# Kernel optimization log

Hardware: AMD Instinct MI355X
Metric: run time of the kernel (lower is better)

Reference implementation:

```python
import jax, jax.numpy as jnp
import numpy as np

GROUPS = 32
EPS = 1e-5


def group_norm(x, gamma, beta):
    # x: [B,H,W,C], channels_last, groups over channel dim (Keras GroupNormalization default)
    B, H, W, C = x.shape
    xg = x.reshape(B, H, W, GROUPS, C // GROUPS)
    mean = xg.mean(axis=(1, 2, 4), keepdims=True)
    var = xg.var(axis=(1, 2, 4), keepdims=True)
    xn = ((xg - mean) * jax.lax.rsqrt(var + EPS)).reshape(B, H, W, C)
    return xn * gamma + beta


def conv1x1(x, w, b):
    # 1x1 conv == per-pixel dense: [B,H,W,C] x [C,D] -> [B,H,W,D]
    return jnp.einsum('bhwc,cd->bhwd', x, w) + b


def setup_inputs() -> dict:
    key = jax.random.key(0)
    ks = jax.random.split(key, 10)
    C = 512
    s = 1.0 / np.sqrt(C)
    inp = {
        'x': jax.random.normal(ks[0], (2, 64, 64, C), dtype=jnp.float32),
        'gamma': jnp.ones((C,), jnp.float32),
        'beta': jnp.zeros((C,), jnp.float32),
        'wq': jax.random.normal(ks[1], (C, C), jnp.float32) * s,
        'bq': jnp.zeros((C,), jnp.float32),
        'wk': jax.random.normal(ks[2], (C, C), jnp.float32) * s,
        'bk': jnp.zeros((C,), jnp.float32),
        'wv': jax.random.normal(ks[3], (C, C), jnp.float32) * s,
        'bv': jnp.zeros((C,), jnp.float32),
        'wp': jax.random.normal(ks[4], (C, C), jnp.float32) * s,
        'bp': jnp.zeros((C,), jnp.float32),
    }
    return inp


def reference(x, gamma, beta, wq, bq, wk, bk, wv, bv, wp, bp):
    B, H, W, C = x.shape
    N = H * W
    xn = group_norm(x, gamma, beta)
    q = conv1x1(xn, wq, bq).reshape(B, N, C)
    k = conv1x1(xn, wk, bk).reshape(B, N, C)
    v = conv1x1(xn, wv, bv).reshape(B, N, C)
    scale = 1.0 / jnp.sqrt(jnp.asarray(C, x.dtype))
    scores = jnp.einsum('bnc,bmc->bnm', q, k) * scale  # [B,N,N]
    attn = jax.nn.softmax(scores, axis=-1)
    out = jnp.einsum('bnm,bmc->bnc', attn, v).reshape(B, H, W, C)
    return conv1x1(out, wp, bp) + x
```

## Files before the change

kernel.cpp:

```cpp
#include <hip/hip_runtime.h>
#include <hip/hip_fp16.h>

typedef _Float16 half_t;
typedef _Float16 half8 __attribute__((ext_vector_type(8)));
typedef float floatx4 __attribute__((ext_vector_type(4)));

static constexpr int BATCH = 2;
static constexpr int NSP = 4096;
static constexpr int CH = 512;
static constexpr int NQKV = 3 * CH;

static constexpr size_t OFF_STATS = 0;
static constexpr size_t OFF_ROWSUM = 512;
static constexpr size_t OFF_WQKV = 36864;
static constexpr size_t WQKV_BYTES = (size_t)NQKV * CH * 2;
static constexpr size_t OFF_WP = OFF_WQKV + WQKV_BYTES;
static constexpr size_t WP_BYTES = (size_t)CH * CH * 2;
static constexpr size_t OFF_XN = OFF_WP + WP_BYTES;
static constexpr size_t XN_BYTES = (size_t)BATCH * NSP * CH * 2;
static constexpr size_t OFF_QKV = OFF_XN + XN_BYTES;
static constexpr size_t QKV_BYTES = (size_t)BATCH * NSP * NQKV * 2;
static constexpr size_t OFF_VT = OFF_QKV + QKV_BYTES;
static constexpr size_t OFF_AO = OFF_VT + XN_BYTES;
static constexpr size_t OFF_S = OFF_AO + XN_BYTES;
static constexpr size_t S_BYTES_1 = (size_t)NSP * NSP * 2;

__device__ __forceinline__ void gld16(void* lds, const void* g) {
  __builtin_amdgcn_global_load_lds(
      (__attribute__((address_space(1))) void*)(g),
      (__attribute__((address_space(3))) void*)(lds),
      16, 0, 0);
}

__global__ void zero4(floatx4* p, long n4) {
  long i = (long)blockIdx.x * 256 + threadIdx.x;
  if (i < n4) p[i] = floatx4{0.f, 0.f, 0.f, 0.f};
}

__global__ __launch_bounds__(256) void gn_stats(const float* __restrict__ x,
                                                float* __restrict__ st) {
  int b = blockIdx.y;
  int tid = (int)threadIdx.x;
  int c0 = (tid * 4) & (CH - 1);
  int g = c0 >> 4;
  const float* base = x + (long)b * NSP * CH + (long)blockIdx.x * 16 * CH + tid * 4;
  float s = 0.f, s2 = 0.f;
#pragma unroll
  for (int it = 0; it < 8; ++it) {
    floatx4 v = *(const floatx4*)(base + (long)it * 1024);
#pragma unroll
    for (int r = 0; r < 4; ++r) { s += v[r]; s2 += v[r] * v[r]; }
  }
  __shared__ float gs[32], gs2[32];
  if (tid < 32) { gs[tid] = 0.f; gs2[tid] = 0.f; }
  __syncthreads();
  atomicAdd(&gs[g], s);
  atomicAdd(&gs2[g], s2);
  __syncthreads();
  if (tid < 32) {
    atomicAdd(&st[(b * 32 + tid) * 2], gs[tid]);
    atomicAdd(&st[(b * 32 + tid) * 2 + 1], gs2[tid]);
  }
}

__global__ void gn_finalize(float* st) {
  int bg = threadIdx.x;
  float s = st[bg * 2], s2 = st[bg * 2 + 1];
  const float inv = 1.f / 65536.f;
  float mean = s * inv;
  float var = s2 * inv - mean * mean;
  st[bg * 2] = mean;
  st[bg * 2 + 1] = rsqrtf(var + 1e-5f);
}

__global__ __launch_bounds__(256) void gn_apply(const float* __restrict__ x,
                                                const float* __restrict__ st,
                                                const float* __restrict__ gamma,
                                                const float* __restrict__ beta,
                                                half_t* __restrict__ xn) {
  long i = ((long)blockIdx.x * 256 + threadIdx.x) * 8;
  int c = (int)(i & (CH - 1));
  int b = (int)(i >> 21);
  int g = c >> 4;
  float mean = st[((b << 5) + g) * 2];
  float rstd = st[((b << 5) + g) * 2 + 1];
  floatx4 a = *(const floatx4*)(x + i);
  floatx4 d = *(const floatx4*)(x + i + 4);
  half8 o;
#pragma unroll
  for (int r = 0; r < 4; ++r) {
    o[r]     = (half_t)((a[r] - mean) * rstd * gamma[c + r] + beta[c + r]);
    o[r + 4] = (half_t)((d[r] - mean) * rstd * gamma[c + r + 4] + beta[c + r + 4]);
  }
  *(half8*)(xn + i) = o;
}

__global__ __launch_bounds__(256) void transpose_w(
    const float* __restrict__ w0, const float* __restrict__ w1,
    const float* __restrict__ w2, const float* __restrict__ w3,
    half_t* __restrict__ o0, half_t* __restrict__ o1,
    half_t* __restrict__ o2, half_t* __restrict__ o3) {
  const float* w; half_t* o;
  switch (blockIdx.z) {
    case 0: w = w0; o = o0; break;
    case 1: w = w1; o = o1; break;
    case 2: w = w2; o = o2; break;
    default: w = w3; o = o3; break;
  }
  __shared__ float t[32][33];
  int d0 = blockIdx.x * 32, c0 = blockIdx.y * 32;
  int tx = threadIdx.x & 31, ty = threadIdx.x >> 5;
#pragma unroll
  for (int i = 0; i < 4; ++i)
    t[ty + i * 8][tx] = w[(long)(c0 + ty + i * 8) * CH + d0 + tx];
  __syncthreads();
#pragma unroll
  for (int i = 0; i < 4; ++i) {
    int d = ty + i * 8;
    o[(long)(d0 + d) * CH + c0 + tx] = (half_t)t[tx][d];
  }
}

__global__ __launch_bounds__(256) void transpose_v(const half_t* __restrict__ v,
                                                   half_t* __restrict__ vt) {
  __shared__ half_t t[32][33];
  int b = blockIdx.z;
  int d0 = blockIdx.x * 32, n0 = blockIdx.y * 32;
  int tx = threadIdx.x & 31, ty = threadIdx.x >> 5;
  const half_t* vb = v + (long)b * NSP * NQKV;
  half_t* ob = vt + (long)b * NSP * CH;
#pragma unroll
  for (int i = 0; i < 4; ++i)
    t[ty + i * 8][tx] = vb[(long)(n0 + ty + i * 8) * NQKV + d0 + tx];
  __syncthreads();
#pragma unroll
  for (int i = 0; i < 4; ++i) {
    int d = ty + i * 8;
    ob[(long)(d0 + d) * NSP + n0 + tx] = t[tx][d];
  }
}

template <int BM, int BN, int BK, int EPI, int SWZ, typename OutT>
__global__ __launch_bounds__(256) void gemm_nt(
    const half_t* __restrict__ X, const half_t* __restrict__ Y,
    OutT* __restrict__ Co, const float* __restrict__ b0,
    const float* __restrict__ b1, const float* __restrict__ b2,
    const float* __restrict__ resid, float* __restrict__ rowsum,
    int M, int N, int K, int ldx, int ldy, int ldc,
    long xbs, long ybs, long cbs, float scale) {
  constexpr int SM = BM / 32;
  constexpr int SN = BN / 32;
  constexpr int ROWS = BM + BN;
  constexpr int CPR = BK / 8;
  constexpr int RPW = 64 / CPR;
  constexpr int ROUNDS = (ROWS * BK * 2) / 4096;
  constexpr int KSTEPS = BK / 32;
  static_assert(BM % (4 * RPW) == 0, "no As/Bs straddle within a round");
  __shared__ __align__(16) half_t Sh[ROWS * BK];
  half_t* As = Sh;
  half_t* Bs = Sh + BM * BK;

  const int zb = blockIdx.z;
  int bx, by;
  if (SWZ) {
    int lin = (int)(blockIdx.x + gridDim.x * blockIdx.y);
    int wmt = 256 / (int)gridDim.x;
    by = wmt * (lin >> 8) + ((lin & 255) % wmt);
    bx = (lin & 255) / wmt;
  } else {
    bx = blockIdx.x;
    by = blockIdx.y;
  }

  const half_t* Xb = X + (long)zb * xbs;
  const half_t* Yb = Y + (long)zb * ybs;
  OutT* Cb = Co + (long)zb * cbs;

  const int m0 = by * BM;
  const int n0 = bx * BN;
  const int tid = (int)threadIdx.x;
  const int wave = tid >> 6;
  const int lane = tid & 63;
  const int quad = lane >> 4;
  const int l16 = lane & 15;
  const int wm = wave >> 1;
  const int wn = wave & 1;

  floatx4 acc[SM][SN] = {};

  const int srow = lane / CPR;
  const int schunk = lane % CPR;

  for (int k0 = 0; k0 < K; k0 += BK) {
#pragma unroll
    for (int r = 0; r < ROUNDS; ++r) {
      int row = r * (4 * RPW) + wave * RPW + srow;
      int gchunk = schunk ^ (row & (CPR - 1));
      const char* src;
      if (row < BM)
        src = (const char*)(Xb + (long)(m0 + row) * ldx + k0) + gchunk * 16;
      else
        src = (const char*)(Yb + (long)(n0 + row - BM) * ldy + k0) + gchunk * 16;
      gld16((char*)Sh + (r * 4 + wave) * 1024, src);
    }
    __syncthreads();

#pragma unroll
    for (int kk = 0; kk < KSTEPS; ++kk) {
      half8 af[SM], bf[SN];
#pragma unroll
      for (int i = 0; i < SM; ++i) {
        int m = wm * (BM / 2) + i * 16 + l16;
        int cc = (kk * 4 + quad) ^ (m & (CPR - 1));
        af[i] = *(const half8*)(As + m * BK + cc * 8);
      }
#pragma unroll
      for (int j = 0; j < SN; ++j) {
        int n = wn * (BN / 2) + j * 16 + l16;
        int cc = (kk * 4 + quad) ^ (n & (CPR - 1));
        bf[j] = *(const half8*)(Bs + n * BK + cc * 8);
      }
#pragma unroll
      for (int i = 0; i < SM; ++i)
#pragma unroll
        for (int j = 0; j < SN; ++j)
          acc[i][j] = __builtin_amdgcn_mfma_f32_16x16x32_f16(af[i], bf[j], acc[i][j], 0, 0, 0);
    }
    __syncthreads();
  }

#pragma unroll
  for (int i = 0; i < SM; ++i) {
    int gmb = m0 + wm * (BM / 2) + i * 16 + quad * 4;
    float rs[4] = {0.f, 0.f, 0.f, 0.f};
    float inv[4];
    if (EPI == 4) {
#pragma unroll
      for (int r = 0; r < 4; ++r)
        inv[r] = 1.f / rowsum[(long)zb * NSP + gmb + r];
    }
#pragma unroll
    for (int j = 0; j < SN; ++j) {
      int gn = n0 + wn * (BN / 2) + j * 16 + l16;
      float bias = 0.f, sc = 1.f;
      if (EPI == 1) {
        if (gn < CH) { bias = b0[gn]; sc = scale; }
        else if (gn < 2 * CH) { bias = b1[gn - CH]; }
        else { bias = b2[gn - 2 * CH]; }
      } else if (EPI == 2) {
        bias = b0[gn];
      }
#pragma unroll
      for (int r = 0; r < 4; ++r) {
        long idx = (long)(gmb + r) * ldc + gn;
        float v = acc[i][j][r];
        if (EPI == 1) v = (v + bias) * sc;
        if (EPI == 2) v = v + bias + resid[idx];
        if (EPI == 3) { v = __expf(v); rs[r] += v; }
        if (EPI == 4) v *= inv[r];
        Cb[idx] = (OutT)v;
      }
    }
    if (EPI == 3) {
#pragma unroll
      for (int r = 0; r < 4; ++r) {
        float v = rs[r];
        v += __shfl_xor(v, 1);
        v += __shfl_xor(v, 2);
        v += __shfl_xor(v, 4);
        v += __shfl_xor(v, 8);
        if (l16 == 0) atomicAdd(&rowsum[(long)zb * NSP + gmb + r], v);
      }
    }
  }
}

extern "C" void kernel_launch(void* const* d_in, const int* in_sizes, int n_in,
                              void* d_out, int out_size, void* d_ws, size_t ws_size,
                              hipStream_t stream) {
  const float* x = (const float*)d_in[0];
  const float* gamma = (const float*)d_in[1];
  const float* beta = (const float*)d_in[2];
  const float* wq = (const float*)d_in[3];
  const float* bq = (const float*)d_in[4];
  const float* wk = (const float*)d_in[5];
  const float* bk = (const float*)d_in[6];
  const float* wv = (const float*)d_in[7];
  const float* bv = (const float*)d_in[8];
  const float* wp = (const float*)d_in[9];
  const float* bp = (const float*)d_in[10];
  float* out = (float*)d_out;
  char* ws = (char*)d_ws;

  float* st = (float*)(ws + OFF_STATS);
  float* rsum = (float*)(ws + OFF_ROWSUM);
  half_t* wqkvT = (half_t*)(ws + OFF_WQKV);
  half_t* wpT = (half_t*)(ws + OFF_WP);
  half_t* xn = (half_t*)(ws + OFF_XN);
  half_t* qkv = (half_t*)(ws + OFF_QKV);
  half_t* vt = (half_t*)(ws + OFF_VT);
  half_t* ao = (half_t*)(ws + OFF_AO);
  half_t* S = (half_t*)(ws + OFF_S);

  half_t* q = qkv;
  half_t* k = qkv + CH;
  half_t* v = qkv + 2 * CH;

  const float scale = 0.044194173824159216f;
  const long bQKV = (long)NSP * NQKV;
  const long bNC = (long)NSP * CH;
  const long bNN = (long)NSP * NSP;

  zero4<<<9, 256, 0, stream>>>((floatx4*)st, 2080);
  gn_stats<<<dim3(256, BATCH), 256, 0, stream>>>(x, st);
  gn_finalize<<<1, 64, 0, stream>>>(st);
  gn_apply<<<2048, 256, 0, stream>>>(x, st, gamma, beta, xn);
  transpose_w<<<dim3(16, 16, 4), 256, 0, stream>>>(
      wq, wk, wv, wp, wqkvT, wqkvT + (size_t)CH * CH, wqkvT + 2 * (size_t)CH * CH, wpT);

  gemm_nt<128, 128, 64, 1, 0, half_t><<<dim3(NQKV / 128, BATCH * NSP / 128, 1), 256, 0, stream>>>(
      xn, wqkvT, qkv, bq, bk, bv, nullptr, nullptr, BATCH * NSP, NQKV, CH,
      CH, CH, NQKV, 0, 0, 0, scale);
  transpose_v<<<dim3(16, 128, BATCH), 256, 0, stream>>>(v, vt);

  bool full = ws_size >= OFF_S + 2 * S_BYTES_1;
  if (full) {
    gemm_nt<128, 128, 64, 3, 1, half_t><<<dim3(32, 32, BATCH), 256, 0, stream>>>(
        q, k, S, nullptr, nullptr, nullptr, nullptr, rsum, NSP, NSP, CH,
        NQKV, NQKV, NSP, bQKV, bQKV, bNN, 1.f);
    gemm_nt<64, 64, 128, 4, 1, half_t><<<dim3(CH / 64, NSP / 64, BATCH), 256, 0, stream>>>(
        S, vt, ao, nullptr, nullptr, nullptr, nullptr, rsum, NSP, CH, NSP,
        NSP, NSP, CH, bNN, bNC, bNC, 1.f);
  } else {
    for (int bb = 0; bb < BATCH; ++bb) {
      gemm_nt<128, 128, 64, 3, 1, half_t><<<dim3(32, 32, 1), 256, 0, stream>>>(
          q + bb * bQKV, k + bb * bQKV, S, nullptr, nullptr, nullptr, nullptr,
          rsum + bb * NSP, NSP, NSP, CH, NQKV, NQKV, NSP, 0, 0, 0, 1.f);
      gemm_nt<64, 64, 128, 4, 1, half_t><<<dim3(CH / 64, NSP / 64, 1), 256, 0, stream>>>(
          S, vt + bb * bNC, ao + bb * bNC, nullptr, nullptr, nullptr, nullptr,
          rsum + bb * NSP, NSP, CH, NSP, NSP, NSP, CH, 0, 0, 0, 1.f);
    }
  }
  gemm_nt<64, 64, 128, 2, 0, float><<<dim3(CH / 64, BATCH * NSP / 64, 1), 256, 0, stream>>>(
      ao, wpT, out, bp, nullptr, nullptr, x, nullptr, BATCH * NSP, CH, CH,
      CH, CH, CH, 0, 0, 0, 1.f);
}
```

Baseline: 273.2 us.

## Double-buffer LDS tiles in GEMM and retune tile shapes for CPR=8

Measured after the change: 316.8 us. 1.16x slower.

```diff
diff --git a/kernel.cpp b/kernel.cpp
--- a/kernel.cpp
+++ b/kernel.cpp
@@ -155,10 +155,10 @@
   constexpr int RPW = 64 / CPR;
   constexpr int ROUNDS = (ROWS * BK * 2) / 4096;
   constexpr int KSTEPS = BK / 32;
+  constexpr int BUF = ROWS * BK;
   static_assert(BM % (4 * RPW) == 0, "no As/Bs straddle within a round");
-  __shared__ __align__(16) half_t Sh[ROWS * BK];
-  half_t* As = Sh;
-  half_t* Bs = Sh + BM * BK;
+  static_assert(CPR == 8, "CPR=8 is the conflict-free LDS config");
+  __shared__ __align__(16) half_t Sh[2 * BUF];
 
   const int zb = blockIdx.z;
   int bx, by;
@@ -190,21 +190,36 @@
 
   const int srow = lane / CPR;
   const int schunk = lane % CPR;
+  const char* Xc = (const char*)Xb;
+
+  int soff[ROUNDS];
+#pragma unroll
+  for (int r = 0; r < ROUNDS; ++r) {
+    int row = r * (4 * RPW) + wave * RPW + srow;
+    int gchunk = schunk ^ (row & (CPR - 1));
+    const char* p = (row < BM)
+        ? (const char*)(Xb + (long)(m0 + row) * ldx)
+        : (const char*)(Yb + (long)(n0 + row - BM) * ldy);
+    soff[r] = (int)(p + gchunk * 16 - Xc);
+  }
+
+  half_t* cur = Sh;
+  half_t* nxt = Sh + BUF;
+#pragma unroll
+  for (int r = 0; r < ROUNDS; ++r)
+    gld16((char*)cur + (r * 4 + wave) * 1024, Xc + (long)soff[r]);
 
   for (int k0 = 0; k0 < K; k0 += BK) {
-#pragma unroll
-    for (int r = 0; r < ROUNDS; ++r) {
-      int row = r * (4 * RPW) + wave * RPW + srow;
-      int gchunk = schunk ^ (row & (CPR - 1));
-      const char* src;
-      if (row < BM)
-        src = (const char*)(Xb + (long)(m0 + row) * ldx + k0) + gchunk * 16;
-      else
-        src = (const char*)(Yb + (long)(n0 + row - BM) * ldy + k0) + gchunk * 16;
-      gld16((char*)Sh + (r * 4 + wave) * 1024, src);
-    }
     __syncthreads();
-
+    if (k0 + BK < K) {
+#pragma unroll
+      for (int r = 0; r < ROUNDS; ++r) {
+        soff[r] += BK * 2;
+        gld16((char*)nxt + (r * 4 + wave) * 1024, Xc + (long)soff[r]);
+      }
+    }
+    half_t* As = cur;
+    half_t* Bs = cur + BM * BK;
 #pragma unroll
     for (int kk = 0; kk < KSTEPS; ++kk) {
       half8 af[SM], bf[SN];
@@ -226,7 +241,7 @@
         for (int j = 0; j < SN; ++j)
           acc[i][j] = __builtin_amdgcn_mfma_f32_16x16x32_f16(af[i], bf[j], acc[i][j], 0, 0, 0);
     }
-    __syncthreads();
+    half_t* t = cur; cur = nxt; nxt = t;
   }
 
 #pragma unroll
@@ -318,30 +333,30 @@
   transpose_w<<<dim3(16, 16, 4), 256, 0, stream>>>(
       wq, wk, wv, wp, wqkvT, wqkvT + (size_t)CH * CH, wqkvT + 2 * (size_t)CH * CH, wpT);
 
-  gemm_nt<128, 128, 64, 1, 0, half_t><<<dim3(NQKV / 128, BATCH * NSP / 128, 1), 256, 0, stream>>>(
+  gemm_nt<128, 64, 64, 1, 0, half_t><<<dim3(NQKV / 64, BATCH * NSP / 128, 1), 256, 0, stream>>>(
       xn, wqkvT, qkv, bq, bk, bv, nullptr, nullptr, BATCH * NSP, NQKV, CH,
       CH, CH, NQKV, 0, 0, 0, scale);
   transpose_v<<<dim3(16, 128, BATCH), 256, 0, stream>>>(v, vt);
 
   bool full = ws_size >= OFF_S + 2 * S_BYTES_1;
   if (full) {
-    gemm_nt<128, 128, 64, 3, 1, half_t><<<dim3(32, 32, BATCH), 256, 0, stream>>>(
+    gemm_nt<128, 64, 64, 3, 1, half_t><<<dim3(NSP / 64, NSP / 128, BATCH), 256, 0, stream>>>(
         q, k, S, nullptr, nullptr, nullptr, nullptr, rsum, NSP, NSP, CH,
         NQKV, NQKV, NSP, bQKV, bQKV, bNN, 1.f);
-    gemm_nt<64, 64, 128, 4, 1, half_t><<<dim3(CH / 64, NSP / 64, BATCH), 256, 0, stream>>>(
+    gemm_nt<64, 64, 64, 4, 1, half_t><<<dim3(CH / 64, NSP / 64, BATCH), 256, 0, stream>>>(
         S, vt, ao, nullptr, nullptr, nullptr, nullptr, rsum, NSP, CH, NSP,
         NSP, NSP, CH, bNN, bNC, bNC, 1.f);
   } else {
     for (int bb = 0; bb < BATCH; ++bb) {
-      gemm_nt<128, 128, 64, 3, 1, half_t><<<dim3(32, 32, 1), 256, 0, stream>>>(
+      gemm_nt<128, 64, 64, 3, 1, half_t><<<dim3(NSP / 64, NSP / 128, 1), 256, 0, stream>>>(
           q + bb * bQKV, k + bb * bQKV, S, nullptr, nullptr, nullptr, nullptr,
           rsum + bb * NSP, NSP, NSP, CH, NQKV, NQKV, NSP, 0, 0, 0, 1.f);
-      gemm_nt<64, 64, 128, 4, 1, half_t><<<dim3(CH / 64, NSP / 64, 1), 256, 0, stream>>>(
+      gemm_nt<64, 64, 64, 4, 1, half_t><<<dim3(CH / 64, NSP / 64, 1), 256, 0, stream>>>(
           S, vt + bb * bNC, ao + bb * bNC, nullptr, nullptr, nullptr, nullptr,
           rsum + bb * NSP, NSP, CH, NSP, NSP, NSP, CH, 0, 0, 0, 1.f);
     }
   }
-  gemm_nt<64, 64, 128, 2, 0, float><<<dim3(CH / 64, BATCH * NSP / 64, 1), 256, 0, stream>>>(
+  gemm_nt<64, 64, 64, 2, 0, float><<<dim3(CH / 64, BATCH * NSP / 64, 1), 256, 0, stream>>>(
       ao, wpT, out, bp, nullptr, nullptr, x, nullptr, BATCH * NSP, CH, CH,
       CH, CH, CH, 0, 0, 0, 1.f);
 }
```
